# Kernel tuning notes

Hardware: AMD Instinct MI355X
Metric: run time of the kernel (lower is better)

## Reference

```python
import jax, jax.numpy as jnp
import numpy as np

TEMP = 20.0     # args.temp
ATT_WT = 0.3    # args.att_wt
EPS = 1e-12     # torch F.normalize eps

L, B, C, H, W = 3, 2, 2048, 60, 60   # 3 layer4 bottleneck maps
CH = 256                              # merged feature channels for f_q/f_s


def setup_inputs() -> dict:
    key = jax.random.key(0)
    k1, k2, k3, k4, k5 = jax.random.split(key, 5)
    return {
        "fq_feats": jax.random.normal(k1, (L, B, C, H, W), dtype=jnp.float32),
        "fs_feats": jax.random.normal(k2, (L, B, C, H, W), dtype=jnp.float32),
        "f_q": jax.random.normal(k3, (B, CH, H, W), dtype=jnp.float32),
        "f_s": jax.random.normal(k4, (B, CH, H, W), dtype=jnp.float32),
        "corr_weight": jax.random.normal(k5, (L,), dtype=jnp.float32),
    }


def _l2_normalize(x, axis):
    # torch F.normalize(dim=1): x / max(||x||, eps)
    n = jnp.sqrt(jnp.sum(x * x, axis=axis, keepdims=True))
    return x / jnp.maximum(n, EPS)


def reference(fq_feats, fs_feats, f_q, f_s, corr_weight):
    b, ch, h, w = f_q.shape
    hw = h * w
    # per-scale channel-wise L2 normalize (cosine correlation)
    fqn = _l2_normalize(fq_feats, axis=2)   # [L,B,C,H,W]
    fsn = _l2_normalize(fs_feats, axis=2)
    # get_corr: pairwise cosine similarity volume per scale -> [B, L, hw_q, hw_s]
    fq_flat = fqn.reshape(fqn.shape[0], b, fqn.shape[2], hw)  # [L,B,C,hw]
    fs_flat = fsn.reshape(fsn.shape[0], b, fsn.shape[2], hw)
    corr = jnp.einsum('lbcq,lbcs->blqs', fq_flat, fs_flat)    # [B,L,hw,hw]
    # MatchNet corr_forward: 1x1 conv reducing match_ch -> 1, softmax over
    # support positions (scaled by temp), attend into v = f_s
    red = jnp.einsum('l,blqs->bqs', corr_weight, corr)        # [B,hw,hw]
    attn = jax.nn.softmax(red * TEMP, axis=-1)                # over support hw
    v = f_s.reshape(b, ch, hw)                                # [B,ch,hw]
    att_fq = jnp.einsum('bqs,bcs->bcq', attn, v).reshape(b, ch, h, w)
    fq = (f_q + att_fq * ATT_WT) / (1.0 + ATT_WT)
    return fq, att_fq
```

## Files before the change

### kernel.cpp

```cpp
#include <hip/hip_runtime.h>
#include <hip/hip_bf16.h>
#include <stdint.h>

#define L3D 3
#define BD 2
#define CD 2048
#define HW 3600
#define CH 256
#define HWP 3712
#define KD 6144
#define SP 3712
#define LB6 6
#define NPLANE 12

typedef __attribute__((ext_vector_type(8))) short short8;
typedef __attribute__((ext_vector_type(4))) float f32x4;
typedef __attribute__((ext_vector_type(2))) long i64x2;
typedef long i64;

__device__ __forceinline__ short f2bf(float v) {
  uint32_t x = __float_as_uint(v);
  uint32_t r = (x + 0x7FFFu + ((x >> 16) & 1u)) >> 16;
  return (short)(r & 0xFFFFu);
}

__device__ __forceinline__ void load_lds16(const void* g, void* l) {
  __builtin_amdgcn_global_load_lds(
      (const __attribute__((address_space(1))) void*)g,
      (__attribute__((address_space(3))) void*)l, 16, 0, 0);
}

__global__ __launch_bounds__(256) void norm1_k(const float* __restrict__ fq,
                                               const float* __restrict__ fs,
                                               float* __restrict__ partial) {
  const int j = blockIdx.y;
  const int p = blockIdx.z;
  const float* x = (j < LB6) ? (fq + (size_t)j * CD * HW)
                             : (fs + (size_t)(j - LB6) * CD * HW);
  const int tid = threadIdx.x;
  const int q = blockIdx.x * 64 + (tid & 63);
  const int sub = tid >> 6;
  float s0 = 0.f, s1 = 0.f, s2 = 0.f, s3 = 0.f;
  if (q < HW) {
    const float* pp = x + ((size_t)p * 512 + (size_t)sub * 128) * HW + q;
    for (int c = 0; c < 128; c += 4) {
      float v0 = pp[(size_t)(c + 0) * HW];
      float v1 = pp[(size_t)(c + 1) * HW];
      float v2 = pp[(size_t)(c + 2) * HW];
      float v3 = pp[(size_t)(c + 3) * HW];
      s0 += v0 * v0; s1 += v1 * v1; s2 += v2 * v2; s3 += v3 * v3;
    }
  }
  __shared__ float buf[256];
  buf[tid] = (s0 + s1) + (s2 + s3);
  __syncthreads();
  if (tid < 64 && q < HW) {
    float t = buf[tid] + buf[tid + 64] + buf[tid + 128] + buf[tid + 192];
    partial[((size_t)p * NPLANE + j) * HW + q] = t;
  }
}

__global__ __launch_bounds__(256) void norm2_k(const float* __restrict__ partial,
                                               float* __restrict__ invn) {
  const int idx = blockIdx.x * 256 + threadIdx.x;
  if (idx >= NPLANE * HW) return;
  const size_t st = (size_t)NPLANE * HW;
  float t = partial[idx] + partial[st + idx] + partial[2 * st + idx] + partial[3 * st + idx];
  invn[idx] = 1.f / fmaxf(sqrtf(t), 1e-12f);
}

__global__ __launch_bounds__(256) void nt_k(const float* __restrict__ x,
                                            const float* __restrict__ invn,
                                            const float* __restrict__ cw,
                                            uint8_t* __restrict__ dst,
                                            int usew) {
  const int lb = blockIdx.z;
  const int l = lb / BD;
  const int b = lb % BD;
  const int qt = blockIdx.x * 64;
  const int ct = blockIdx.y * 64;
  const int tid = threadIdx.x;
  __shared__ float tile[64][65];

  const int tx = tid & 63, ty = tid >> 6;
  const float* px = x + ((size_t)lb * CD + ct) * HW;
  const int q = qt + tx;
#pragma unroll
  for (int r = 0; r < 16; r++) {
    int cl = r * 4 + ty;
    tile[cl][tx] = (q < HW) ? px[(size_t)cl * HW + q] : 0.f;
  }
  __syncthreads();

  const float scale = usew ? (cw[l] * 32.0f) : 32.0f;
  const int wx = tid & 7, wy = tid >> 3;
  const int pos = (wx & 3) * 2 + (wx >> 2);
#pragma unroll
  for (int it = 0; it < 2; it++) {
    int qrow = wy + it * 32;
    int qq = qt + qrow;
    if (qq < HW) {
      float iv = invn[(size_t)lb * HW + qq] * scale;
      float v[8];
#pragma unroll
      for (int j = 0; j < 8; j++) v[j] = tile[wx * 8 + j][qrow] * iv;
      int lo = 0, hi = 0;
      lo = __builtin_amdgcn_cvt_pk_fp8_f32(v[0], v[1], lo, false);
      lo = __builtin_amdgcn_cvt_pk_fp8_f32(v[2], v[3], lo, true);
      hi = __builtin_amdgcn_cvt_pk_fp8_f32(v[4], v[5], hi, false);
      hi = __builtin_amdgcn_cvt_pk_fp8_f32(v[6], v[7], hi, true);
      int2 pk = make_int2(lo, hi);
      *reinterpret_cast<int2*>(dst + ((size_t)b * HWP + qq) * KD +
                               (size_t)l * CD + ct + pos * 8) = pk;
    }
  }
}

__global__ __launch_bounds__(256, 2) void gemm_main(const uint8_t* __restrict__ A,
                                                    const uint8_t* __restrict__ B,
                                                    __hip_bfloat16* __restrict__ C) {
  const int bz = blockIdx.z;
  const int m0 = blockIdx.y * 128;
  const int n0 = blockIdx.x * 128;
  const int tid = threadIdx.x;
  const int lane = tid & 63;
  const int wv = tid >> 6;

  __shared__ uint8_t lA[128 * 64];
  __shared__ uint8_t lB[128 * 64];

  const uint8_t* gA = A + (size_t)bz * HWP * KD;
  const uint8_t* gB = B + (size_t)bz * HWP * KD;

  const int r0 = tid >> 2;
  const int kc = (tid & 3) * 16;
  const int wb = (tid & ~63) * 16;

  const int wr = (wv >> 1) * 64;
  const int wc = (wv & 1) * 64;
  const int ml = lane & 15;
  const int kq = (lane >> 4) * 16;

  f32x4 acc[4][4];
#pragma unroll
  for (int i = 0; i < 4; i++)
#pragma unroll
    for (int j = 0; j < 4; j++) acc[i][j] = (f32x4){0.f, 0.f, 0.f, 0.f};

  for (int k0 = 0; k0 < KD; k0 += 64) {
    const uint8_t* pa0 = gA + (size_t)(m0 + r0) * KD + k0 + kc;
    const uint8_t* pb0 = gB + (size_t)(n0 + r0) * KD + k0 + kc;
    load_lds16(pa0, &lA[wb]);
    load_lds16(pa0 + (size_t)64 * KD, &lA[wb + 4096]);
    load_lds16(pb0, &lB[wb]);
    load_lds16(pb0 + (size_t)64 * KD, &lB[wb + 4096]);
    __syncthreads();

    i64 a0[4], a1[4], b0[4], b1[4];
#pragma unroll
    for (int t = 0; t < 4; t++) {
      i64x2 av = *reinterpret_cast<const i64x2*>(&lA[(wr + t * 16 + ml) * 64 + kq]);
      i64x2 bv = *reinterpret_cast<const i64x2*>(&lB[(wc + t * 16 + ml) * 64 + kq]);
      a0[t] = av[0]; a1[t] = av[1];
      b0[t] = bv[0]; b1[t] = bv[1];
    }
#pragma unroll
    for (int mt = 0; mt < 4; mt++)
#pragma unroll
      for (int nt = 0; nt < 4; nt++) {
        acc[mt][nt] = __builtin_amdgcn_mfma_f32_16x16x32_fp8_fp8(a0[mt], b0[nt], acc[mt][nt], 0, 0, 0);
        acc[mt][nt] = __builtin_amdgcn_mfma_f32_16x16x32_fp8_fp8(a1[mt], b1[nt], acc[mt][nt], 0, 0, 0);
      }
    __syncthreads();
  }

  __hip_bfloat16* oc = C + (size_t)bz * HWP * SP;
  const int rq = (lane >> 4) * 4;
  const int cl = lane & 15;
#pragma unroll
  for (int mt = 0; mt < 4; mt++) {
    const int rb = m0 + wr + mt * 16 + rq;
#pragma unroll
    for (int nt = 0; nt < 4; nt++) {
      const int col = n0 + wc + nt * 16 + cl;
      f32x4 v = acc[mt][nt];
#pragma unroll
      for (int r = 0; r < 4; r++) {
        const int rr = rb + r;
        if (rr < HW) *reinterpret_cast<short*>(&oc[(size_t)rr * SP + col]) = f2bf(v[r]);
      }
    }
  }
}

__global__ __launch_bounds__(256) void softmax_k(const __hip_bfloat16* __restrict__ red,
                                                 __hip_bfloat16* __restrict__ attn) {
  const int q = blockIdx.x;
  const int b = blockIdx.y;
  const __hip_bfloat16* row = red + ((size_t)b * HWP + q) * SP;
  __hip_bfloat16* orow = attn + ((size_t)b * HWP + q) * SP;
  const int tid = threadIdx.x;
  const int lane = tid & 63, wv = tid >> 6;
  const float SM = 20.0f / 1024.0f;

  float r[15];
  float mx = -3.4e38f;
#pragma unroll
  for (int i = 0; i < 15; i++) {
    int s = i * 256 + tid;
    float v = (s < HW) ? __bfloat162float(row[s]) : -3.4e38f;
    r[i] = v;
    mx = fmaxf(mx, v);
  }
  for (int off = 32; off > 0; off >>= 1) mx = fmaxf(mx, __shfl_down(mx, off, 64));
  __shared__ float sm[4];
  if (lane == 0) sm[wv] = mx;
  __syncthreads();
  mx = fmaxf(fmaxf(sm[0], sm[1]), fmaxf(sm[2], sm[3]));

  float sum = 0.f;
#pragma unroll
  for (int i = 0; i < 15; i++) {
    int s = i * 256 + tid;
    float e = (s < HW) ? __expf((r[i] - mx) * SM) : 0.f;
    r[i] = e;
    sum += e;
  }
  for (int off = 32; off > 0; off >>= 1) sum += __shfl_down(sum, off, 64);
  __syncthreads();
  if (lane == 0) sm[wv] = sum;
  __syncthreads();
  const float inv = 1.f / (sm[0] + sm[1] + sm[2] + sm[3]);

#pragma unroll
  for (int i = 0; i < 15; i++) {
    int s = i * 256 + tid;
    if (s < SP) *reinterpret_cast<short*>(&orow[s]) = f2bf(r[i] * inv);
  }
}

__global__ __launch_bounds__(256) void castv_k(const float* __restrict__ fs,
                                               __hip_bfloat16* __restrict__ vb) {
  const int idx = blockIdx.x * 256 + threadIdx.x;
  if (idx >= BD * CH * SP) return;
  const int s = idx % SP;
  const int bc = idx / SP;
  float v = (s < HW) ? fs[(size_t)bc * HW + s] : 0.f;
  *reinterpret_cast<short*>(&vb[idx]) = f2bf(v);
}

__global__ __launch_bounds__(256, 2) void pv_gemm(const __hip_bfloat16* __restrict__ A,
                                                  const __hip_bfloat16* __restrict__ B,
                                                  const float* __restrict__ fqin,
                                                  float* __restrict__ out) {
  const int bz = blockIdx.z;
  const int m0 = blockIdx.y * 128;
  const int n0 = blockIdx.x * 64;
  const int tid = threadIdx.x;
  const int lane = tid & 63;
  const int wv = tid >> 6;

  __shared__ __hip_bfloat16 lA[128 * 32];
  __shared__ __hip_bfloat16 lB[64 * 32];

  const __hip_bfloat16* gA = A + (size_t)bz * CH * SP;
  const __hip_bfloat16* gB = B + (size_t)bz * HWP * SP;

  const int r0 = tid >> 2;
  const int kc = (tid & 3) * 8;
  const int wb = (tid & ~63) * 8;

  const int wr = (wv >> 1) * 64;
  const int wc = (wv & 1) * 32;
  const int ml = lane & 15;
  const int kq = (lane >> 4) * 8;

  f32x4 acc[4][2];
#pragma unroll
  for (int i = 0; i < 4; i++)
#pragma unroll
    for (int j = 0; j < 2; j++) acc[i][j] = (f32x4){0.f, 0.f, 0.f, 0.f};

  for (int k0 = 0; k0 < SP; k0 += 32) {
    const __hip_bfloat16* pa0 = gA + (size_t)(m0 + r0) * SP + k0 + kc;
    const __hip_bfloat16* pb0 = gB + (size_t)(n0 + r0) * SP + k0 + kc;
    load_lds16(pa0, &lA[wb]);
    load_lds16(pa0 + (size_t)64 * SP, &lA[wb + 2048]);
    load_lds16(pb0, &lB[wb]);
    __syncthreads();

    short8 af[4], bfr[2];
#pragma unroll
    for (int t = 0; t < 4; t++)
      af[t] = *reinterpret_cast<const short8*>(&lA[(wr + t * 16 + ml) * 32 + kq]);
#pragma unroll
    for (int t = 0; t < 2; t++)
      bfr[t] = *reinterpret_cast<const short8*>(&lB[(wc + t * 16 + ml) * 32 + kq]);
#pragma unroll
    for (int mt = 0; mt < 4; mt++)
#pragma unroll
      for (int nt = 0; nt < 2; nt++)
        acc[mt][nt] = __builtin_amdgcn_mfma_f32_16x16x32_bf16(af[mt], bfr[nt], acc[mt][nt], 0, 0, 0);
    __syncthreads();
  }

  const size_t obase = (size_t)bz * CH * HW;
  const size_t attoff = (size_t)BD * CH * HW;
  const int rq = (lane >> 4) * 4;
  const int cl = lane & 15;
#pragma unroll
  for (int mt = 0; mt < 4; mt++) {
    const int rb = m0 + wr + mt * 16 + rq;
#pragma unroll
    for (int nt = 0; nt < 2; nt++) {
      const int col = n0 + wc + nt * 16 + cl;
      if (col < HW) {
        f32x4 v = acc[mt][nt];
#pragma unroll
        for (int r = 0; r < 4; r++) {
          const int c = rb + r;
          size_t oi = obase + (size_t)c * HW + col;
          float att = v[r];
          out[oi] = (fqin[oi] + 0.3f * att) * (1.0f / 1.3f);
          out[attoff + oi] = att;
        }
      }
    }
  }
}

extern "C" void kernel_launch(void* const* d_in, const int* in_sizes, int n_in,
                              void* d_out, int out_size, void* d_ws, size_t ws_size,
                              hipStream_t stream) {
  const float* fqf = (const float*)d_in[0];
  const float* fsf = (const float*)d_in[1];
  const float* f_q = (const float*)d_in[2];
  const float* f_s = (const float*)d_in[3];
  const float* cw  = (const float*)d_in[4];
  float* out = (float*)d_out;

  char* w = (char*)d_ws;
  float* partial = (float*)w;  w += ((size_t)4 * NPLANE * HW * 4 + 255) & ~(size_t)255;
  float* invn = (float*)w;     w += ((size_t)NPLANE * HW * 4 + 255) & ~(size_t)255;
  uint8_t* An = (uint8_t*)w;   w += (size_t)BD * HWP * KD;
  uint8_t* Bn = (uint8_t*)w;   w += (size_t)BD * HWP * KD;
  __hip_bfloat16* red = (__hip_bfloat16*)w;
  __hip_bfloat16* attn = (__hip_bfloat16*)An;
  __hip_bfloat16* vb = (__hip_bfloat16*)(An + (size_t)BD * HWP * SP * 2);
  float* invq = invn;
  float* invs = invn + (size_t)LB6 * HW;
  (void)ws_size; (void)in_sizes; (void)n_in; (void)out_size;

  norm1_k<<<dim3(57, NPLANE, 4), 256, 0, stream>>>(fqf, fsf, partial);
  norm2_k<<<(NPLANE * HW + 255) / 256, 256, 0, stream>>>(partial, invn);
  nt_k<<<dim3(57, 32, LB6), 256, 0, stream>>>(fqf, invq, cw, An, 1);
  nt_k<<<dim3(57, 32, LB6), 256, 0, stream>>>(fsf, invs, cw, Bn, 0);
  gemm_main<<<dim3(29, 29, BD), 256, 0, stream>>>(An, Bn, red);
  softmax_k<<<dim3(HW, BD), 256, 0, stream>>>(red, attn);
  castv_k<<<(BD * CH * SP + 255) / 256, 256, 0, stream>>>(f_s, vb);
  pv_gemm<<<dim3(58, 2, BD), 256, 0, stream>>>(vb, attn, f_q, out);
}
```

Measured before the change: 869.8 us.

## Fuse norm and fp8 transpose kernels; use scaled 16x16x128 fp8 MFMA with swizzled LDS

```diff
diff --git a/kernel.cpp b/kernel.cpp
--- a/kernel.cpp
+++ b/kernel.cpp
@@ -15,8 +15,8 @@
 
 typedef __attribute__((ext_vector_type(8))) short short8;
 typedef __attribute__((ext_vector_type(4))) float f32x4;
-typedef __attribute__((ext_vector_type(2))) long i64x2;
-typedef long i64;
+typedef __attribute__((ext_vector_type(4))) int i32x4;
+typedef __attribute__((ext_vector_type(8))) int i32x8;
 
 __device__ __forceinline__ short f2bf(float v) {
   uint32_t x = __float_as_uint(v);
@@ -30,88 +30,73 @@
       (__attribute__((address_space(3))) void*)l, 16, 0, 0);
 }
 
-__global__ __launch_bounds__(256) void norm1_k(const float* __restrict__ fq,
-                                               const float* __restrict__ fs,
-                                               float* __restrict__ partial) {
+__global__ __launch_bounds__(256) void fnt_k(const float* __restrict__ fq,
+                                             const float* __restrict__ fs,
+                                             const float* __restrict__ cw,
+                                             uint8_t* __restrict__ An,
+                                             uint8_t* __restrict__ Bn) {
   const int j = blockIdx.y;
-  const int p = blockIdx.z;
-  const float* x = (j < LB6) ? (fq + (size_t)j * CD * HW)
-                             : (fs + (size_t)(j - LB6) * CD * HW);
+  const int qt = blockIdx.x * 64;
+  const bool isq = (j < LB6);
+  const int lb = isq ? j : j - LB6;
+  const int l = lb / BD, b = lb % BD;
+  const float* x = (isq ? fq : fs) + (size_t)lb * CD * HW;
+  uint8_t* dst = isq ? An : Bn;
+
   const int tid = threadIdx.x;
-  const int q = blockIdx.x * 64 + (tid & 63);
-  const int sub = tid >> 6;
+  const int tx = tid & 63, part = tid >> 6;
+  const int q = qt + tx;
+
   float s0 = 0.f, s1 = 0.f, s2 = 0.f, s3 = 0.f;
   if (q < HW) {
-    const float* pp = x + ((size_t)p * 512 + (size_t)sub * 128) * HW + q;
-    for (int c = 0; c < 128; c += 4) {
-      float v0 = pp[(size_t)(c + 0) * HW];
-      float v1 = pp[(size_t)(c + 1) * HW];
-      float v2 = pp[(size_t)(c + 2) * HW];
-      float v3 = pp[(size_t)(c + 3) * HW];
+    const float* p = x + (size_t)part * 512 * HW + q;
+    for (int c = 0; c < 512; c += 4) {
+      float v0 = p[(size_t)(c + 0) * HW];
+      float v1 = p[(size_t)(c + 1) * HW];
+      float v2 = p[(size_t)(c + 2) * HW];
+      float v3 = p[(size_t)(c + 3) * HW];
       s0 += v0 * v0; s1 += v1 * v1; s2 += v2 * v2; s3 += v3 * v3;
     }
   }
   __shared__ float buf[256];
+  __shared__ float ivs[64];
   buf[tid] = (s0 + s1) + (s2 + s3);
   __syncthreads();
-  if (tid < 64 && q < HW) {
+  if (tid < 64) {
     float t = buf[tid] + buf[tid + 64] + buf[tid + 128] + buf[tid + 192];
-    partial[((size_t)p * NPLANE + j) * HW + q] = t;
-  }
-}
-
-__global__ __launch_bounds__(256) void norm2_k(const float* __restrict__ partial,
-                                               float* __restrict__ invn) {
-  const int idx = blockIdx.x * 256 + threadIdx.x;
-  if (idx >= NPLANE * HW) return;
-  const size_t st = (size_t)NPLANE * HW;
-  float t = partial[idx] + partial[st + idx] + partial[2 * st + idx] + partial[3 * st + idx];
-  invn[idx] = 1.f / fmaxf(sqrtf(t), 1e-12f);
-}
-
-__global__ __launch_bounds__(256) void nt_k(const float* __restrict__ x,
-                                            const float* __restrict__ invn,
-                                            const float* __restrict__ cw,
-                                            uint8_t* __restrict__ dst,
-                                            int usew) {
-  const int lb = blockIdx.z;
-  const int l = lb / BD;
-  const int b = lb % BD;
-  const int qt = blockIdx.x * 64;
-  const int ct = blockIdx.y * 64;
-  const int tid = threadIdx.x;
+    const float scale = isq ? (cw[l] * 32.0f) : 32.0f;
+    ivs[tid] = (1.f / fmaxf(sqrtf(t), 1e-12f)) * scale;
+  }
+
   __shared__ float tile[64][65];
-
-  const int tx = tid & 63, ty = tid >> 6;
-  const float* px = x + ((size_t)lb * CD + ct) * HW;
-  const int q = qt + tx;
-#pragma unroll
-  for (int r = 0; r < 16; r++) {
-    int cl = r * 4 + ty;
-    tile[cl][tx] = (q < HW) ? px[(size_t)cl * HW + q] : 0.f;
-  }
-  __syncthreads();
-
-  const float scale = usew ? (cw[l] * 32.0f) : 32.0f;
   const int wx = tid & 7, wy = tid >> 3;
-  const int pos = (wx & 3) * 2 + (wx >> 2);
-#pragma unroll
-  for (int it = 0; it < 2; it++) {
-    int qrow = wy + it * 32;
-    int qq = qt + qrow;
-    if (qq < HW) {
-      float iv = invn[(size_t)lb * HW + qq] * scale;
-      float v[8];
-#pragma unroll
-      for (int j = 0; j < 8; j++) v[j] = tile[wx * 8 + j][qrow] * iv;
-      int lo = 0, hi = 0;
-      lo = __builtin_amdgcn_cvt_pk_fp8_f32(v[0], v[1], lo, false);
-      lo = __builtin_amdgcn_cvt_pk_fp8_f32(v[2], v[3], lo, true);
-      hi = __builtin_amdgcn_cvt_pk_fp8_f32(v[4], v[5], hi, false);
-      hi = __builtin_amdgcn_cvt_pk_fp8_f32(v[6], v[7], hi, true);
-      int2 pk = make_int2(lo, hi);
-      *reinterpret_cast<int2*>(dst + ((size_t)b * HWP + qq) * KD +
-                               (size_t)l * CD + ct + pos * 8) = pk;
+  for (int ct = 0; ct < 32; ct++) {
+    const float* px = x + (size_t)ct * 64 * HW;
+    __syncthreads();
+#pragma unroll
+    for (int r = 0; r < 16; r++) {
+      int cl = r * 4 + part;
+      tile[cl][tx] = (q < HW) ? px[(size_t)cl * HW + q] : 0.f;
+    }
+    __syncthreads();
+#pragma unroll
+    for (int it = 0; it < 2; it++) {
+      int qrow = wy + it * 32;
+      int qq = qt + qrow;
+      if (qq < HW) {
+        float iv = ivs[qrow];
+        float v[8];
+#pragma unroll
+        for (int jj = 0; jj < 8; jj++) v[jj] = tile[wx * 8 + jj][qrow] * iv;
+        int lo = 0, hi = 0;
+        lo = __builtin_amdgcn_cvt_pk_fp8_f32(v[0], v[1], lo, false);
+        lo = __builtin_amdgcn_cvt_pk_fp8_f32(v[2], v[3], lo, true);
+        hi = __builtin_amdgcn_cvt_pk_fp8_f32(v[4], v[5], hi, false);
+        hi = __builtin_amdgcn_cvt_pk_fp8_f32(v[6], v[7], hi, true);
+        int2 pk = make_int2(lo, hi);
+        *reinterpret_cast<int2*>(dst + ((size_t)b * HWP + qq) * KD +
+                                 (size_t)l * CD + ct * 64 + wx * 8) = pk;
+      }
     }
   }
 }
@@ -119,58 +104,73 @@
 __global__ __launch_bounds__(256, 2) void gemm_main(const uint8_t* __restrict__ A,
                                                     const uint8_t* __restrict__ B,
                                                     __hip_bfloat16* __restrict__ C) {
-  const int bz = blockIdx.z;
-  const int m0 = blockIdx.y * 128;
-  const int n0 = blockIdx.x * 128;
+  const int bz = blockIdx.y;
+  const int lin = blockIdx.x;
+  int m_t, n_t;
+  if (lin < 812) { int g = lin / 116, r = lin % 116; m_t = g * 4 + (r & 3); n_t = r >> 2; }
+  else           { m_t = 28; n_t = lin - 812; }
+  const int m0 = m_t * 128, n0 = n_t * 128;
   const int tid = threadIdx.x;
   const int lane = tid & 63;
   const int wv = tid >> 6;
 
-  __shared__ uint8_t lA[128 * 64];
-  __shared__ uint8_t lB[128 * 64];
+  __shared__ uint8_t lA[128 * 128];
+  __shared__ uint8_t lB[128 * 128];
 
   const uint8_t* gA = A + (size_t)bz * HWP * KD;
   const uint8_t* gB = B + (size_t)bz * HWP * KD;
 
-  const int r0 = tid >> 2;
-  const int kc = (tid & 3) * 16;
-  const int wb = (tid & ~63) * 16;
+  const int r_loc = tid >> 3;
+  const int slot = tid & 7;
+  const int csw = (slot - r_loc) & 7;
+  const int wavebase = (tid & ~63) * 16;
 
   const int wr = (wv >> 1) * 64;
   const int wc = (wv & 1) * 64;
   const int ml = lane & 15;
-  const int kq = (lane >> 4) * 16;
+  const int kg = lane >> 4;
 
   f32x4 acc[4][4];
 #pragma unroll
   for (int i = 0; i < 4; i++)
 #pragma unroll
-    for (int j = 0; j < 4; j++) acc[i][j] = (f32x4){0.f, 0.f, 0.f, 0.f};
-
-  for (int k0 = 0; k0 < KD; k0 += 64) {
-    const uint8_t* pa0 = gA + (size_t)(m0 + r0) * KD + k0 + kc;
-    const uint8_t* pb0 = gB + (size_t)(n0 + r0) * KD + k0 + kc;
-    load_lds16(pa0, &lA[wb]);
-    load_lds16(pa0 + (size_t)64 * KD, &lA[wb + 4096]);
-    load_lds16(pb0, &lB[wb]);
-    load_lds16(pb0 + (size_t)64 * KD, &lB[wb + 4096]);
-    __syncthreads();
-
-    i64 a0[4], a1[4], b0[4], b1[4];
+    for (int jj = 0; jj < 4; jj++) acc[i][jj] = (f32x4){0.f, 0.f, 0.f, 0.f};
+
+  for (int k0 = 0; k0 < KD; k0 += 128) {
+#pragma unroll
+    for (int i = 0; i < 4; i++) {
+      load_lds16(gA + (size_t)(m0 + i * 32 + r_loc) * KD + k0 + csw * 16,
+                 &lA[i * 4096 + wavebase]);
+      load_lds16(gB + (size_t)(n0 + i * 32 + r_loc) * KD + k0 + csw * 16,
+                 &lB[i * 4096 + wavebase]);
+    }
+    __syncthreads();
+
+    i32x8 af[4], bf[4];
 #pragma unroll
     for (int t = 0; t < 4; t++) {
-      i64x2 av = *reinterpret_cast<const i64x2*>(&lA[(wr + t * 16 + ml) * 64 + kq]);
-      i64x2 bv = *reinterpret_cast<const i64x2*>(&lB[(wc + t * 16 + ml) * 64 + kq]);
-      a0[t] = av[0]; a1[t] = av[1];
-      b0[t] = bv[0]; b1[t] = bv[1];
+      {
+        const int row = wr + t * 16 + ml;
+        const int base = row << 7;
+        i32x4 lo = *reinterpret_cast<const i32x4*>(&lA[base + (((kg * 2)     + row) & 7) * 16]);
+        i32x4 hi = *reinterpret_cast<const i32x4*>(&lA[base + (((kg * 2 + 1) + row) & 7) * 16]);
+        af[t] = __builtin_shufflevector(lo, hi, 0, 1, 2, 3, 4, 5, 6, 7);
+      }
+      {
+        const int row = wc + t * 16 + ml;
+        const int base = row << 7;
+        i32x4 lo = *reinterpret_cast<const i32x4*>(&lB[base + (((kg * 2)     + row) & 7) * 16]);
+        i32x4 hi = *reinterpret_cast<const i32x4*>(&lB[base + (((kg * 2 + 1) + row) & 7) * 16]);
+        bf[t] = __builtin_shufflevector(lo, hi, 0, 1, 2, 3, 4, 5, 6, 7);
+      }
     }
 #pragma unroll
     for (int mt = 0; mt < 4; mt++)
 #pragma unroll
-      for (int nt = 0; nt < 4; nt++) {
-        acc[mt][nt] = __builtin_amdgcn_mfma_f32_16x16x32_fp8_fp8(a0[mt], b0[nt], acc[mt][nt], 0, 0, 0);
-        acc[mt][nt] = __builtin_amdgcn_mfma_f32_16x16x32_fp8_fp8(a1[mt], b1[nt], acc[mt][nt], 0, 0, 0);
-      }
+      for (int nt = 0; nt < 4; nt++)
+        acc[mt][nt] = __builtin_amdgcn_mfma_scale_f32_16x16x128_f8f6f4(
+            af[mt], bf[nt], acc[mt][nt], 0, 0,
+            0, 0x7F7F7F7F, 0, 0x7F7F7F7F);
     __syncthreads();
   }
 
@@ -279,7 +279,7 @@
 #pragma unroll
   for (int i = 0; i < 4; i++)
 #pragma unroll
-    for (int j = 0; j < 2; j++) acc[i][j] = (f32x4){0.f, 0.f, 0.f, 0.f};
+    for (int jj = 0; jj < 2; jj++) acc[i][jj] = (f32x4){0.f, 0.f, 0.f, 0.f};
 
   for (int k0 = 0; k0 < SP; k0 += 32) {
     const __hip_bfloat16* pa0 = gA + (size_t)(m0 + r0) * SP + k0 + kc;
@@ -340,22 +340,15 @@
   float* out = (float*)d_out;
 
   char* w = (char*)d_ws;
-  float* partial = (float*)w;  w += ((size_t)4 * NPLANE * HW * 4 + 255) & ~(size_t)255;
-  float* invn = (float*)w;     w += ((size_t)NPLANE * HW * 4 + 255) & ~(size_t)255;
   uint8_t* An = (uint8_t*)w;   w += (size_t)BD * HWP * KD;
   uint8_t* Bn = (uint8_t*)w;   w += (size_t)BD * HWP * KD;
   __hip_bfloat16* red = (__hip_bfloat16*)w;
   __hip_bfloat16* attn = (__hip_bfloat16*)An;
   __hip_bfloat16* vb = (__hip_bfloat16*)(An + (size_t)BD * HWP * SP * 2);
-  float* invq = invn;
-  float* invs = invn + (size_t)LB6 * HW;
   (void)ws_size; (void)in_sizes; (void)n_in; (void)out_size;
 
-  norm1_k<<<dim3(57, NPLANE, 4), 256, 0, stream>>>(fqf, fsf, partial);
-  norm2_k<<<(NPLANE * HW + 255) / 256, 256, 0, stream>>>(partial, invn);
-  nt_k<<<dim3(57, 32, LB6), 256, 0, stream>>>(fqf, invq, cw, An, 1);
-  nt_k<<<dim3(57, 32, LB6), 256, 0, stream>>>(fsf, invs, cw, Bn, 0);
-  gemm_main<<<dim3(29, 29, BD), 256, 0, stream>>>(An, Bn, red);
+  fnt_k<<<dim3(57, NPLANE), 256, 0, stream>>>(fqf, fsf, cw, An, Bn);
+  gemm_main<<<dim3(841, BD), 256, 0, stream>>>(An, Bn, red);
   softmax_k<<<dim3(HW, BD), 256, 0, stream>>>(red, attn);
   castv_k<<<(BD * CH * SP + 255) / 256, 256, 0, stream>>>(f_s, vb);
   pv_gemm<<<dim3(58, 2, BD), 256, 0, stream>>>(vb, attn, f_q, out);
```

After: 861.7 us. About the same (-0.9%).
